# Optimization experiments

Measured on AMD Instinct MI355X. Metric: run time of the kernel, lower is better.

The kernel has to match this reference:

```python
import jax, jax.numpy as jnp
import numpy as np

N_EMBD = 768
N_HEAD = 12
HEAD_DIM = N_EMBD // N_HEAD  # 64


def setup_inputs() -> dict:
    key = jax.random.key(0)
    k1, k2, k3 = jax.random.split(key, 3)
    B, S = 4, 2048
    x = jax.random.normal(k1, (B, S, N_EMBD), dtype=jnp.float32)
    W_attn = jax.random.normal(k2, (N_EMBD, 3 * N_EMBD), dtype=jnp.float32) * 0.02
    b_attn = jax.random.normal(k3, (3 * N_EMBD,), dtype=jnp.float32) * 0.02
    return {"x": x, "W_attn": W_attn, "b_attn": b_attn}


def reference(x, W_attn, b_attn):
    B, S, E = x.shape
    H, D = N_HEAD, HEAD_DIM
    # fused QKV projection (torch Linear: x @ W^T + b; here W_attn stored as [E, 3E])
    qkv = x @ W_attn + b_attn  # [B, S, 3E]
    q, k, v = jnp.split(qkv, 3, axis=-1)
    q = q.reshape(B, S, H, D)
    k = k.reshape(B, S, H, D)
    v = v.reshape(B, S, H, D)
    scale = 1.0 / np.sqrt(D).astype(np.float32)
    scores = jnp.einsum('bqhd,bkhd->bhqk', q, k) * scale  # [B, H, S, S]
    causal = jnp.tril(jnp.ones((S, S), dtype=bool))
    # ReLU attention nonlinearity (no softmax); masked entries -> 0
    att = jnp.where(causal, jnp.maximum(scores, 0.0), 0.0)
    y = jnp.einsum('bhqk,bkhd->bqhd', att, v)  # [B, S, H, D]
    return y.reshape(B, S, E)
```

## Files before the change

### kernel.cpp

```cpp
#include <hip/hip_runtime.h>

typedef __attribute__((ext_vector_type(8))) short short8;
typedef __attribute__((ext_vector_type(4))) float floatx4;
typedef __attribute__((ext_vector_type(4))) unsigned int uint4v;

#define S_LEN 2048
#define NH 12
#define HD 64
#define EMB 768
#define E3 2304

#define MF(a, b, c) __builtin_amdgcn_mfma_f32_16x16x32_bf16(a, b, c, 0, 0, 0)

__device__ __forceinline__ unsigned short f2bf(float f) {
    unsigned int u = __builtin_bit_cast(unsigned int, f);
    u += 0x7FFFu + ((u >> 16) & 1u);
    return (unsigned short)(u >> 16);
}

__device__ __forceinline__ unsigned int pack2bf(float a, float b) {
#if __has_builtin(__builtin_amdgcn_cvt_pk_bf16_f32)
    typedef __attribute__((ext_vector_type(2))) short short2v;
    short2v r = __builtin_amdgcn_cvt_pk_bf16_f32(a, b);
    return __builtin_bit_cast(unsigned int, r);
#else
    return (unsigned int)f2bf(a) | ((unsigned int)f2bf(b) << 16);
#endif
}

__device__ __forceinline__ void pl32_swap(unsigned int& x, unsigned int& y) {
#if __has_builtin(__builtin_amdgcn_permlane32_swap)
    typedef __attribute__((ext_vector_type(2))) unsigned int uint2v_;
    uint2v_ r = __builtin_amdgcn_permlane32_swap(x, y, false, false);
    x = r[0]; y = r[1];
#else
    asm("v_permlane32_swap_b32 %0, %1" : "+v"(x), "+v"(y));
#endif
}
__device__ __forceinline__ void pl16_swap(unsigned int& x, unsigned int& y) {
#if __has_builtin(__builtin_amdgcn_permlane16_swap)
    typedef __attribute__((ext_vector_type(2))) unsigned int uint2v_;
    uint2v_ r = __builtin_amdgcn_permlane16_swap(x, y, false, false);
    x = r[0]; y = r[1];
#else
    asm("v_permlane16_swap_b32 %0, %1" : "+v"(x), "+v"(y));
#endif
}

__device__ __forceinline__ void gl_lds16(const void* g, void* l) {
    __builtin_amdgcn_global_load_lds(
        (const __attribute__((address_space(1))) unsigned int*)g,
        (__attribute__((address_space(3))) unsigned int*)l, 16, 0, 0);
}

__global__ __launch_bounds__(256) void conv_fused(const float* __restrict__ x,
                                                  ushort* __restrict__ xb,
                                                  const float* __restrict__ W,
                                                  ushort* __restrict__ Wt) {
    int tid = threadIdx.x;
    if (blockIdx.x < 6144) {
        int i = (blockIdx.x * 256 + tid) * 4;
        float4 f = *(const float4*)(x + i);
        ushort4 o;
        o.x = f2bf(f.x); o.y = f2bf(f.y); o.z = f2bf(f.z); o.w = f2bf(f.w);
        *(ushort4*)(xb + i) = o;
    } else {
        __shared__ float tile[32][33];
        int b2 = blockIdx.x - 6144;
        int n0 = (b2 % 72) * 32, k0 = (b2 / 72) * 32;
        int tx = tid & 31, ty = tid >> 5;
        for (int i = 0; i < 4; i++)
            tile[ty + i * 8][tx] = W[(size_t)(k0 + ty + i * 8) * E3 + n0 + tx];
        __syncthreads();
        for (int i = 0; i < 4; i++)
            Wt[(size_t)(n0 + ty + i * 8) * EMB + k0 + tx] = f2bf(tile[tx][ty + i * 8]);
    }
}

__global__ __launch_bounds__(512, 1) void qkv_gemm(const ushort* __restrict__ Xb,
                                                   const ushort* __restrict__ Wt,
                                                   const float* __restrict__ bias,
                                                   ushort* __restrict__ QKb,
                                                   ushort* __restrict__ Vt) {
    extern __shared__ char ldsb[];
    const int tid  = threadIdx.x;
    const int w = tid >> 6, lane = tid & 63;
    const int l15 = lane & 15, quad = lane >> 4;
    const int r8 = lane >> 3, cc = lane & 7;
    const int wm = w >> 1, wn = w & 1;
    const int m0 = blockIdx.x * 256, n0 = blockIdx.y * 128;

    floatx4 acc[4][4] = {};

    const char* agp = (const char*)Xb + (size_t)(m0 + w * 32 + r8) * 1536 + (cc ^ r8) * 16;
    const char* bgp = (const char*)Wt + (size_t)(n0 + w * 16 + r8) * 1536 + (cc ^ r8) * 16;
    const int adstB = w * 4096;
    const int bdstB = 32768 + w * 2048;

    const int aroB = (wm * 64 + l15) * 128;
    const int broB = 32768 + (wn * 64 + l15) * 128;
    const int swz0 = ((quad) ^ (l15 & 7)) * 16;
    const int swz1 = ((4 + quad) ^ (l15 & 7)) * 16;

    for (int i = 0; i < 4; i++) gl_lds16(agp + i * 12288, ldsb + adstB + i * 1024);
    for (int i = 0; i < 2; i++) gl_lds16(bgp + i * 12288, ldsb + bdstB + i * 1024);
    for (int i = 0; i < 4; i++) gl_lds16(agp + 128 + i * 12288, ldsb + 49152 + adstB + i * 1024);
    for (int i = 0; i < 2; i++) gl_lds16(bgp + 128 + i * 12288, ldsb + 49152 + bdstB + i * 1024);

#pragma unroll
    for (int t = 0; t < 12; ++t) {
        if (t < 11) asm volatile("s_waitcnt vmcnt(6)" ::: "memory");
        else        asm volatile("s_waitcnt vmcnt(0)" ::: "memory");
        __builtin_amdgcn_s_barrier();
        __builtin_amdgcn_sched_barrier(0);

        const char* base = ldsb + (t % 3) * 49152;
        char* sdst = ldsb + ((t + 2) % 3) * 49152;
        const int koff = (t + 2) * 128;
        const bool st = (t < 10);

        short8 af0, af1, bf0, bf1, bf2, bf3;

        af0 = *(const short8*)(base + aroB + 0 * 2048 + swz0);
        af1 = *(const short8*)(base + aroB + 1 * 2048 + swz0);
        bf0 = *(const short8*)(base + broB + 0 * 2048 + swz0);
        bf1 = *(const short8*)(base + broB + 1 * 2048 + swz0);
        bf2 = *(const short8*)(base + broB + 2 * 2048 + swz0);
        bf3 = *(const short8*)(base + broB + 3 * 2048 + swz0);
        if (st) { gl_lds16(agp + koff,         sdst + adstB);
                  gl_lds16(agp + koff + 12288, sdst + adstB + 1024); }
        __builtin_amdgcn_s_setprio(1);
        acc[0][0] = MF(af0, bf0, acc[0][0]); acc[0][1] = MF(af0, bf1, acc[0][1]);
        acc[0][2] = MF(af0, bf2, acc[0][2]); acc[0][3] = MF(af0, bf3, acc[0][3]);
        acc[1][0] = MF(af1, bf0, acc[1][0]); acc[1][1] = MF(af1, bf1, acc[1][1]);
        acc[1][2] = MF(af1, bf2, acc[1][2]); acc[1][3] = MF(af1, bf3, acc[1][3]);
        __builtin_amdgcn_s_setprio(0);
        __builtin_amdgcn_s_barrier();

        af0 = *(const short8*)(base + aroB + 2 * 2048 + swz0);
        af1 = *(const short8*)(base + aroB + 3 * 2048 + swz0);
        if (st) { gl_lds16(agp + koff + 2 * 12288, sdst + adstB + 2048);
                  gl_lds16(agp + koff + 3 * 12288, sdst + adstB + 3072); }
        __builtin_amdgcn_s_setprio(1);
        acc[2][0] = MF(af0, bf0, acc[2][0]); acc[2][1] = MF(af0, bf1, acc[2][1]);
        acc[2][2] = MF(af0, bf2, acc[2][2]); acc[2][3] = MF(af0, bf3, acc[2][3]);
        acc[3][0] = MF(af1, bf0, acc[3][0]); acc[3][1] = MF(af1, bf1, acc[3][1]);
        acc[3][2] = MF(af1, bf2, acc[3][2]); acc[3][3] = MF(af1, bf3, acc[3][3]);
        __builtin_amdgcn_s_setprio(0);
        __builtin_amdgcn_s_barrier();

        af0 = *(const short8*)(base + aroB + 0 * 2048 + swz1);
        af1 = *(const short8*)(base + aroB + 1 * 2048 + swz1);
        bf0 = *(const short8*)(base + broB + 0 * 2048 + swz1);
        bf1 = *(const short8*)(base + broB + 1 * 2048 + swz1);
        bf2 = *(const short8*)(base + broB + 2 * 2048 + swz1);
        bf3 = *(const short8*)(base + broB + 3 * 2048 + swz1);
        if (st) { gl_lds16(bgp + koff,         sdst + bdstB);
                  gl_lds16(bgp + koff + 12288, sdst + bdstB + 1024); }
        __builtin_amdgcn_s_setprio(1);
        acc[0][0] = MF(af0, bf0, acc[0][0]); acc[0][1] = MF(af0, bf1, acc[0][1]);
        acc[0][2] = MF(af0, bf2, acc[0][2]); acc[0][3] = MF(af0, bf3, acc[0][3]);
        acc[1][0] = MF(af1, bf0, acc[1][0]); acc[1][1] = MF(af1, bf1, acc[1][1]);
        acc[1][2] = MF(af1, bf2, acc[1][2]); acc[1][3] = MF(af1, bf3, acc[1][3]);
        __builtin_amdgcn_s_setprio(0);
        __builtin_amdgcn_s_barrier();

        af0 = *(const short8*)(base + aroB + 2 * 2048 + swz1);
        af1 = *(const short8*)(base + aroB + 3 * 2048 + swz1);
        __builtin_amdgcn_s_setprio(1);
        acc[2][0] = MF(af0, bf0, acc[2][0]); acc[2][1] = MF(af0, bf1, acc[2][1]);
        acc[2][2] = MF(af0, bf2, acc[2][2]); acc[2][3] = MF(af0, bf3, acc[2][3]);
        acc[3][0] = MF(af1, bf0, acc[3][0]); acc[3][1] = MF(af1, bf1, acc[3][1]);
        acc[3][2] = MF(af1, bf2, acc[3][2]); acc[3][3] = MF(af1, bf3, acc[3][3]);
        __builtin_amdgcn_s_setprio(0);
    }

    __syncthreads();
    ushort* epi = (ushort*)ldsb;
    int seg = n0 >= 1536 ? 2 : (n0 >= 768 ? 1 : 0);
    if (seg < 2) {
        float scale = (seg == 0) ? 0.125f : 1.0f;
        for (int ni = 0; ni < 4; ni++) {
            int nl = wn * 64 + ni * 16 + l15;
            float bv = bias[n0 + nl];
            for (int mi = 0; mi < 4; mi++)
                for (int r = 0; r < 4; r++) {
                    int ml = wm * 64 + mi * 16 + quad * 4 + r;
                    epi[ml * 132 + nl] = f2bf((acc[mi][ni][r] + bv) * scale);
                }
        }
        __syncthreads();
        int row = tid >> 1, h2 = tid & 1;
        size_t gm = (size_t)(m0 + row);
        for (int i = 0; i < 8; i++) {
            uint4 v = *(const uint4*)&epi[row * 132 + h2 * 64 + i * 8];
            *(uint4*)&QKb[gm * 1536 + n0 + h2 * 64 + i * 8] = v;
        }
    } else {
        for (int ni = 0; ni < 4; ni++) {
            int nl = wn * 64 + ni * 16 + l15;
            float bv = bias[n0 + nl];
            for (int mi = 0; mi < 4; mi++) {
                int ml = wm * 64 + mi * 16 + quad * 4;
                ushort4 p4;
                p4.x = f2bf(acc[mi][ni][0] + bv);
                p4.y = f2bf(acc[mi][ni][1] + bv);
                p4.z = f2bf(acc[mi][ni][2] + bv);
                p4.w = f2bf(acc[mi][ni][3] + bv);
                *(ushort4*)&epi[nl * 264 + ml] = p4;
            }
        }
        __syncthreads();
        int row = tid >> 2, q4 = tid & 3;
        int nn = n0 + row - 1536;
        int hh = nn >> 6, d = nn & 63;
        int bb = m0 >> 11, s0 = m0 & 2047;
        for (int i = 0; i < 8; i++) {
            uint4 v = *(const uint4*)&epi[row * 264 + q4 * 64 + i * 8];
            *(uint4*)&Vt[((size_t)(bb * NH + hh) * HD + d) * S_LEN + s0 + q4 * 64 + i * 8] = v;
        }
    }
}

__global__ __launch_bounds__(256) void attn(const ushort* __restrict__ QKb,
                                            const ushort* __restrict__ Vt,
                                            float* __restrict__ out) {
    __shared__ ushort lds[32768];
    char* ldsb = (char*)lds;
    int tid = threadIdx.x;
    int w = tid >> 6, lane = tid & 63;
    int l15 = lane & 15, quad = lane >> 4;
    int r8 = lane >> 3, cc = lane & 7;
    int rr = lane >> 4;

    int kfo[2];
    for (int ch = 0; ch < 2; ch++)
        kfo[ch] = l15 * 128 + ((ch * 4 + quad) ^ (l15 & 7)) * 16;
    int vfo2[4];
    for (int T = 0; T < 4; T++)
        vfo2[T] = 32768 + l15 * 256 + ((T * 4 + quad) ^ l15) * 16;
    int rhs[2] = { w * 32 + l15, w * 32 + 16 + l15 };
    int kgo = (w * 32 + r8) * 3072 + (cc ^ r8) * 16;
    int vgo[4];
    for (int i = 0; i < 4; i++)
        vgo[i] = (w * 16 + i * 4 + rr) * 4096 + (((lane & 15) ^ ((i * 4 + rr) & 15)) * 16);
    int kst = (w * 32) * 128;
    int vst = 32768 + (w * 16) * 256;

    int b = blockIdx.x;
    int nit, qts[2], bhs[2];
    if (b < 240)      { nit = 1; qts[0] = 15 - b / 48; bhs[0] = b % 48; qts[1] = 0; bhs[1] = 0; }
    else if (b < 480) { int j = b - 240; nit = 2; qts[0] = 10 - j / 48; bhs[0] = j % 48;
                        qts[1] = 1 + j / 48; bhs[1] = j % 48; }
    else              { int j = b - 480; nit = 2; qts[0] = 0; bhs[0] = 2 * j;
                        qts[1] = 0; bhs[1] = 2 * j + 1; }

    const char* kg[2]; const char* vg[2];
    for (int i = 0; i < 2; i++) {
        int bh = bhs[i], bg = bh / NH, h = bh % NH;
        kg[i] = (const char*)(QKb + (size_t)bg * S_LEN * 1536 + 768 + h * 64) + kgo;
        vg[i] = (const char*)(Vt + (size_t)bh * HD * S_LEN);
    }

    auto prefetch = [&](const char* kbase, const char* vbase, int dstP) {
        for (int i = 0; i < 4; i++)
            gl_lds16(kbase + i * 24576, ldsb + dstP * 16384 + kst + i * 1024);
        for (int i = 0; i < 4; i++)
            gl_lds16(vbase + vgo[i], ldsb + dstP * 16384 + vst + i * 1024);
    };

    int p = 0;
    prefetch(kg[0], vg[0], 0);
    for (int ii = 0; ii < nit; ii++) {
        int qt = qts[ii];
        int bh = bhs[ii], bg = bh / NH, h = bh % NH;
        const ushort* Qcol = QKb + (size_t)bg * S_LEN * 1536 + h * 64;
        short8 qf[2][2];
        for (int nq = 0; nq < 2; nq++)
            for (int ch = 0; ch < 2; ch++)
                qf[nq][ch] = *(const short8*)(Qcol +
                    (size_t)(qt * 128 + w * 32 + nq * 16 + l15) * 1536 + ch * 32 + quad * 8);

        floatx4 acco[2][4] = {};
        int nst = qt + 1;
        for (int st = 0; st < nst; st++) {
            __syncthreads();
            if (st + 1 < nst)
                prefetch(kg[ii] + (size_t)(st + 1) * 393216, vg[ii] + (st + 1) * 256, p ^ 1);
            else if (ii + 1 < nit)
                prefetch(kg[ii + 1], vg[ii + 1], p ^ 1);

            bool diag = (st == qt);
            const char* kb = ldsb + p * 16384;

            for (int jsub = 0; jsub < 2; jsub++) {
                floatx4 stc[4][2] = {};
                for (int ch = 0; ch < 2; ch++) {
                    short8 kf[4];
                    for (int mk = 0; mk < 4; mk++)
                        kf[mk] = *(const short8*)(kb + kfo[ch] + jsub * 8192 + mk * 2048);
                    for (int mk = 0; mk < 4; mk++)
                        for (int nq = 0; nq < 2; nq++)
                            stc[mk][nq] = __builtin_amdgcn_mfma_f32_16x16x32_bf16(
                                kf[mk], qf[nq][ch], stc[mk][nq], 0, 0, 0);
                }

                unsigned int pk[4][2][2];
                for (int mk = 0; mk < 4; mk++) {
                    for (int nq = 0; nq < 2; nq++) {
                        float e[4];
                        for (int r = 0; r < 4; r++)
                            e[r] = fmaxf(stc[mk][nq][r], 0.0f);
                        if (diag) {
                            int kl = jsub * 64 + mk * 16 + quad * 4;
                            for (int r = 0; r < 4; r++)
                                if (kl + r > rhs[nq]) e[r] = 0.0f;
                        }
                        pk[mk][nq][0] = pack2bf(e[0], e[1]);
                        pk[mk][nq][1] = pack2bf(e[2], e[3]);
                    }
                }

                for (int pr = 0; pr < 2; pr++) {
                    int T = jsub * 2 + pr;
                    short8 vf[4];
                    for (int ni = 0; ni < 4; ni++)
                        vf[ni] = *(const short8*)(kb + vfo2[T] + ni * 4096);
                    for (int mi = 0; mi < 2; mi++) {
                        unsigned int a0 = pk[2 * pr][mi][0], a1 = pk[2 * pr][mi][1];
                        unsigned int b0 = pk[2 * pr + 1][mi][0], b1 = pk[2 * pr + 1][mi][1];
                        pl32_swap(a0, b0);  pl32_swap(a1, b1);
                        pl16_swap(a0, b0);  pl16_swap(a1, b1);
                        short8 af = __builtin_bit_cast(short8, (uint4v){a0, a1, b0, b1});
                        for (int ni = 0; ni < 4; ni++)
                            acco[mi][ni] = __builtin_amdgcn_mfma_f32_16x16x32_bf16(
                                af, vf[ni], acco[mi][ni], 0, 0, 0);
                    }
                }
            }
            p ^= 1;
        }

        for (int mi = 0; mi < 2; mi++) {
            for (int ni = 0; ni < 4; ni++) {
                int d = ni * 16 + l15;
                for (int r = 0; r < 4; r++) {
                    int s = qt * 128 + w * 32 + mi * 16 + quad * 4 + r;
                    out[((size_t)bg * S_LEN + s) * EMB + h * 64 + d] = acco[mi][ni][r];
                }
            }
        }
    }
}

extern "C" void kernel_launch(void* const* d_in, const int* in_sizes, int n_in,
                              void* d_out, int out_size, void* d_ws, size_t ws_size,
                              hipStream_t stream) {
    const float* x    = (const float*)d_in[0];
    const float* W    = (const float*)d_in[1];
    const float* bias = (const float*)d_in[2];
    float* out = (float*)d_out;

    char* ws = (char*)d_ws;
    const size_t SZ_X  = (size_t)8192 * EMB * 2;
    const size_t SZ_W  = (size_t)E3 * EMB * 2;
    const size_t SZ_QK = (size_t)8192 * 1536 * 2;
    ushort* Xb  = (ushort*)(ws);
    ushort* Wt  = (ushort*)(ws + SZ_X);
    ushort* QKb = (ushort*)(ws + SZ_X + SZ_W);
    ushort* Vt  = (ushort*)(ws + SZ_X + SZ_W + SZ_QK);

    static bool attr_done = false;
    if (!attr_done) {
        hipFuncSetAttribute((const void*)qkv_gemm,
                            hipFuncAttributeMaxDynamicSharedMemorySize, 147456);
        attr_done = true;
    }

    conv_fused<<<dim3(6144 + 1728), dim3(256), 0, stream>>>(x, Xb, W, Wt);
    qkv_gemm<<<dim3(32, 18), dim3(512), 147456, stream>>>(Xb, Wt, bias, QKb, Vt);
    attn<<<dim3(504), dim3(256), 0, stream>>>(QKb, Vt, out);
}
```

Baseline: 186.5 us.

## Rebalance attention work per head and group blocks for K/V locality

```diff
diff --git a/kernel.cpp b/kernel.cpp
--- a/kernel.cpp
+++ b/kernel.cpp
@@ -222,9 +222,9 @@
     }
 }
 
-__global__ __launch_bounds__(256) void attn(const ushort* __restrict__ QKb,
-                                            const ushort* __restrict__ Vt,
-                                            float* __restrict__ out) {
+__global__ __launch_bounds__(256, 2) void attn(const ushort* __restrict__ QKb,
+                                               const ushort* __restrict__ Vt,
+                                               float* __restrict__ out) {
     __shared__ ushort lds[32768];
     char* ldsb = (char*)lds;
     int tid = threadIdx.x;
@@ -248,33 +248,33 @@
     int vst = 32768 + (w * 16) * 256;
 
     int b = blockIdx.x;
-    int nit, qts[2], bhs[2];
-    if (b < 240)      { nit = 1; qts[0] = 15 - b / 48; bhs[0] = b % 48; qts[1] = 0; bhs[1] = 0; }
-    else if (b < 480) { int j = b - 240; nit = 2; qts[0] = 10 - j / 48; bhs[0] = j % 48;
-                        qts[1] = 1 + j / 48; bhs[1] = j % 48; }
-    else              { int j = b - 480; nit = 2; qts[0] = 0; bhs[0] = 2 * j;
-                        qts[1] = 0; bhs[1] = 2 * j + 1; }
-
-    const char* kg[2]; const char* vg[2];
-    for (int i = 0; i < 2; i++) {
-        int bh = bhs[i], bg = bh / NH, h = bh % NH;
-        kg[i] = (const char*)(QKb + (size_t)bg * S_LEN * 1536 + 768 + h * 64) + kgo;
-        vg[i] = (const char*)(Vt + (size_t)bh * HD * S_LEN);
-    }
-
-    auto prefetch = [&](const char* kbase, const char* vbase, int dstP) {
+    int g = b & 7;
+    int idx = b >> 3;
+    int role = idx / 6;
+    int bh = g * 6 + (idx % 6);
+    int nit, qts[2];
+    if (role < 4) { nit = 1; qts[0] = 15 - role; qts[1] = 0; }
+    else          { nit = 2; qts[0] = 15 - role; qts[1] = role - 4; }
+    int bg = bh / NH, h = bh % NH;
+
+    const char* kg = (const char*)(QKb + (size_t)bg * S_LEN * 1536 + 768 + h * 64) + kgo;
+    const char* vgb = (const char*)(Vt + (size_t)bh * HD * S_LEN);
+
+    auto prefetch = [&](int st, int dstP) {
+        const char* kbase = kg + (size_t)st * 393216;
+        const char* vbase = vgb + st * 256;
         for (int i = 0; i < 4; i++)
             gl_lds16(kbase + i * 24576, ldsb + dstP * 16384 + kst + i * 1024);
         for (int i = 0; i < 4; i++)
             gl_lds16(vbase + vgo[i], ldsb + dstP * 16384 + vst + i * 1024);
     };
 
+    const ushort* Qcol = QKb + (size_t)bg * S_LEN * 1536 + h * 64;
+
     int p = 0;
-    prefetch(kg[0], vg[0], 0);
+    prefetch(0, 0);
     for (int ii = 0; ii < nit; ii++) {
         int qt = qts[ii];
-        int bh = bhs[ii], bg = bh / NH, h = bh % NH;
-        const ushort* Qcol = QKb + (size_t)bg * S_LEN * 1536 + h * 64;
         short8 qf[2][2];
         for (int nq = 0; nq < 2; nq++)
             for (int ch = 0; ch < 2; ch++)
@@ -286,9 +286,9 @@
         for (int st = 0; st < nst; st++) {
             __syncthreads();
             if (st + 1 < nst)
-                prefetch(kg[ii] + (size_t)(st + 1) * 393216, vg[ii] + (st + 1) * 256, p ^ 1);
+                prefetch(st + 1, p ^ 1);
             else if (ii + 1 < nit)
-                prefetch(kg[ii + 1], vg[ii + 1], p ^ 1);
+                prefetch(0, p ^ 1);
 
             bool diag = (st == qt);
             const char* kb = ldsb + p * 16384;
@@ -379,5 +379,5 @@
 
     conv_fused<<<dim3(6144 + 1728), dim3(256), 0, stream>>>(x, Xb, W, Wt);
     qkv_gemm<<<dim3(32, 18), dim3(512), 147456, stream>>>(Xb, Wt, bias, QKb, Vt);
-    attn<<<dim3(504), dim3(256), 0, stream>>>(QKb, Vt, out);
-}
+    attn<<<dim3(480), dim3(256), 0, stream>>>(QKb, Vt, out);
+}
```

New measurement: 177.3 us. 4.9% less time.
